# Performance work log

Measured on AMD Instinct MI355X. Metric: run time of the kernel, lower is better.

Reference implementation:

```python
import jax, jax.numpy as jnp
import numpy as np

S, B, LAG, H, F = 10, 16384, 5, 512, 5

def setup_inputs() -> dict:
    key = jax.random.key(0)
    ks = jax.random.split(key, 16)
    sc = 0.05
    inp = {
        'x': jax.random.normal(ks[0], (S, B, LAG), jnp.float32),
        'W_in': jax.random.normal(ks[1], (H, LAG), jnp.float32) * sc,
        'b_in': jax.random.normal(ks[2], (H,), jnp.float32) * sc,
        'Wih0': jax.random.normal(ks[3], (4 * H, H), jnp.float32) * sc,
        'Whh0': jax.random.normal(ks[4], (4 * H, H), jnp.float32) * sc,
        'bih0': jax.random.normal(ks[5], (4 * H,), jnp.float32) * sc,
        'bhh0': jax.random.normal(ks[6], (4 * H,), jnp.float32) * sc,
        'Wih1': jax.random.normal(ks[7], (4 * H, H), jnp.float32) * sc,
        'Whh1': jax.random.normal(ks[8], (4 * H, H), jnp.float32) * sc,
        'bih1': jax.random.normal(ks[9], (4 * H,), jnp.float32) * sc,
        'bhh1': jax.random.normal(ks[10], (4 * H,), jnp.float32) * sc,
        'W_out': jax.random.normal(ks[11], (1, H), jnp.float32) * sc,
        'b_out': jax.random.normal(ks[12], (1,), jnp.float32) * sc,
        'W_f': jax.random.normal(ks[13], (F, H), jnp.float32) * sc,
        'b_f': jax.random.normal(ks[14], (F,), jnp.float32) * sc,
    }
    return inp

def _lstm_cell(g, h, c, Whh, bhh):
    # g: precomputed input-side gates [B,4H]; add recurrent part, PyTorch gate order i,f,g,o
    g = g + h @ Whh.T + bhh
    i, f, gg, o = jnp.split(g, 4, axis=-1)
    c_new = jax.nn.sigmoid(f) * c + jax.nn.sigmoid(i) * jnp.tanh(gg)
    h_new = jax.nn.sigmoid(o) * jnp.tanh(c_new)
    return h_new, c_new

def reference(x, W_in, b_in, Wih0, Whh0, bih0, bhh0, Wih1, Whh1, bih1, bhh1, W_out, b_out, W_f, b_f):
    # input projection for all steps at once: [S,B,H]
    u = x @ W_in.T + b_in
    # precompute input-side LSTM gates for layer 0: [S,B,4H]
    g0_all = u @ Wih0.T + bih0
    zeros = jnp.zeros((B, H), x.dtype)

    def step(carry, g0_t):
        h0, c0, h1, c1 = carry
        h0, c0 = _lstm_cell(g0_t, h0, c0, Whh0, bhh0)
        g1 = h0 @ Wih1.T + bih1  # dropout between layers is eval-mode no-op
        h1, c1 = _lstm_cell(g1, h1, c1, Whh1, bhh1)
        return (h0, c0, h1, c1), h1

    (h0, c0, h1, c1), hs = jax.lax.scan(step, (zeros, zeros, zeros, zeros), g0_all)
    # per-step scalar outputs: [S,B,1] -> [B,S]
    step_out = (hs @ W_out.T + b_out)[:, :, 0].T
    # forecast head from last layer's final hidden state: [B,F]
    fc = h1 @ W_f.T + b_f
    outputs = jnp.concatenate([step_out, fc], axis=1)  # [B, S+F]
    h_n = jnp.stack([h0, h1])  # [2,B,H]
    c_n = jnp.stack([c0, c1])
    return outputs, h_n, c_n
```

## Files before the change

kernel.cpp:

```cpp
#include <hip/hip_runtime.h>
#include <hip/hip_bf16.h>

constexpr int S   = 10;
constexpr int Bsz = 16384;
constexpr int LAG = 5;
constexpr int H   = 512;
constexpr int G4  = 4 * H;
constexpr int F   = 5;
constexpr int BH  = Bsz * H;
constexpr int OUT_HN = Bsz * (S + F);
constexpr int OUT_CN = OUT_HN + 2 * BH;

constexpr int TK   = 32;
constexpr int NBUF = 2;
constexpr int A_T  = 128 * TK;
constexpr int B_T  = 128 * TK;

typedef __attribute__((ext_vector_type(8))) short short8;
typedef __attribute__((ext_vector_type(4))) float f32x4;

__device__ __forceinline__ float sigf(float x) { return 1.0f / (1.0f + __expf(-x)); }
__device__ __forceinline__ float tanh_fast(float x) {
    float e = __expf(2.0f * x);
    return 1.0f - 2.0f / (e + 1.0f);
}

__device__ __forceinline__ void gload_lds16(const void* g, void* l) {
    __builtin_amdgcn_global_load_lds(
        (const __attribute__((address_space(1))) unsigned int*)g,
        (__attribute__((address_space(3))) unsigned int*)l, 16, 0, 0);
}

__global__ __launch_bounds__(256)
void prep_kernel(const float* __restrict__ W_in,  const float* __restrict__ b_in,
                 const float* __restrict__ Wih0,  const float* __restrict__ Whh0,
                 const float* __restrict__ bih0,  const float* __restrict__ bhh0,
                 const float* __restrict__ Wih1,  const float* __restrict__ Whh1,
                 const float* __restrict__ bih1,  const float* __restrict__ bhh1,
                 __hip_bfloat16* __restrict__ W0b, __hip_bfloat16* __restrict__ W1b,
                 float* __restrict__ A0r, float* __restrict__ b0r,
                 float* __restrict__ b1r)
{
    const int r   = blockIdx.x;
    const int tid = threadIdx.x;

    for (int k = tid; k < H; k += 256)
        W0b[r * H + k] = __float2bfloat16(Whh0[r * H + k]);
    for (int k = tid; k < 2 * H; k += 256)
        W1b[r * 2 * H + k] = __float2bfloat16(
            (k < H) ? Wih1[r * H + k] : Whh1[r * H + (k - H)]);

    if (tid < LAG) {
        float s = 0.f;
        for (int h = 0; h < H; ++h) s += Wih0[r * H + h] * W_in[h * LAG + tid];
        A0r[r * LAG + tid] = s;
    } else if (tid == 5) {
        float s = 0.f;
        for (int h = 0; h < H; ++h) s += Wih0[r * H + h] * b_in[h];
        b0r[r] = s + bih0[r] + bhh0[r];
    } else if (tid == 6) {
        b1r[r] = bih1[r] + bhh1[r];
    }
}

__global__ __launch_bounds__(256)
void lstm_gemm(const __hip_bfloat16* __restrict__ Aseg0,
               const __hip_bfloat16* __restrict__ Aseg1,
               int nseg,
               const __hip_bfloat16* __restrict__ W, int ldw,
               const float* __restrict__ bias,
               const float* __restrict__ xs,
               const float* __restrict__ A0r,
               const float* __restrict__ c_in,
               float* __restrict__ c_out,
               float* __restrict__ h32_out,
               __hip_bfloat16* __restrict__ hb16_out,
               int hcol)
{
    __shared__ __align__(16) short As[NBUF * A_T];
    __shared__ __align__(16) short Bs[NBUF * B_T];
    __shared__ float xls[128 * LAG];
    __shared__ float a0ls[128 * LAG];

    const int tid  = threadIdx.x;
    const int lane = tid & 63;
    const int quad = lane >> 4;
    const int li   = lane & 15;
    const int wv   = tid >> 6;
    const int wy   = wv >> 1;
    const int wx   = wv & 1;

    const int l  = blockIdx.y * gridDim.x + blockIdx.x;
    const int v  = (l & 7) * 256 + (l >> 3);
    const int by = v >> 4;
    const int bx = v & 15;
    const int bM_ = by * 128;
    const int cn  = bx * 32;

    const bool has_x = (xs != nullptr);
    if (has_x) {
        for (int i = tid; i < 128 * LAG; i += 256) {
            const int row = i / LAG, ll = i % LAG;
            xls[i] = xs[(size_t)(bM_ + row) * LAG + ll];
        }
        for (int i = tid; i < 128 * LAG; i += 256) {
            const int cl = i / LAG, ll = i % LAG;
            const int r  = (cl >> 5) * H + cn + (cl & 31);
            a0ls[i] = A0r[r * LAG + ll];
        }
        __syncthreads();
    }

    f32x4 acc[4][4];
    #pragma unroll
    for (int i = 0; i < 4; ++i)
        #pragma unroll
        for (int j = 0; j < 4; ++j) acc[i][j] = (f32x4){0.f, 0.f, 0.f, 0.f};

    int a_off[2], w_off[2];
    #pragma unroll
    for (int r = 0; r < 2; ++r) {
        const int idx = r * 256 + tid;
        const int row = idx >> 2;
        const int j   = idx & 3;
        const int js  = j ^ ((row >> 1) & 3);
        a_off[r] = (bM_ + row) * 1024 + js * 8;
        const int rr = (row >> 5) * H + cn + (row & 31);
        w_off[r] = rr * ldw + js * 8;
    }

    const int NT = nseg * 16;

    auto stage_tile = [&](int t) {
        const int seg = t >> 4;
        const int kof = seg * 512 + (t & 15) * TK;
        const short* pa = (const short*)(seg ? Aseg1 : Aseg0) + kof;
        const short* pw = (const short*)W + kof;
        short* as = As + (t & 1) * A_T;
        short* bs = Bs + (t & 1) * B_T;
        #pragma unroll
        for (int r = 0; r < 2; ++r) {
            const int idx = r * 256 + tid;
            gload_lds16(pa + a_off[r], &as[idx * 8]);
            gload_lds16(pw + w_off[r], &bs[idx * 8]);
        }
    };

    const int pch = quad ^ ((li >> 1) & 3);

    auto compute_tile = [&](int t) {
        const short* as = As + (t & 1) * A_T;
        const short* bs = Bs + (t & 1) * B_T;
        short8 af[4], bf[4];
        #pragma unroll
        for (int m = 0; m < 4; ++m)
            af[m] = *(const short8*)&as[(wy * 64 + m * 16 + li) * TK + pch * 8];
        #pragma unroll
        for (int g = 0; g < 4; ++g)
            bf[g] = *(const short8*)&bs[(g * 32 + wx * 16 + li) * TK + pch * 8];
        __builtin_amdgcn_s_setprio(1);
        #pragma unroll
        for (int m = 0; m < 4; ++m)
            #pragma unroll
            for (int g = 0; g < 4; ++g)
                acc[m][g] = __builtin_amdgcn_mfma_f32_16x16x32_bf16(
                    af[m], bf[g], acc[m][g], 0, 0, 0);
        __builtin_amdgcn_s_setprio(0);
    };

    if (NT) {
        stage_tile(0);
        asm volatile("s_waitcnt vmcnt(0)\n\ts_barrier" ::: "memory");
        for (int t = 0; t < NT; ++t) {
            if (t + 1 < NT) stage_tile(t + 1);
            compute_tile(t);
            asm volatile("s_waitcnt vmcnt(0)\n\ts_barrier" ::: "memory");
        }
    }

    const int n = cn + wx * 16 + li;
    float bias4[4], a0reg[4][LAG];
    #pragma unroll
    for (int g = 0; g < 4; ++g) bias4[g] = bias[g * H + n];
    if (has_x) {
        #pragma unroll
        for (int g = 0; g < 4; ++g)
            #pragma unroll
            for (int ll = 0; ll < LAG; ++ll)
                a0reg[g][ll] = a0ls[(g * 32 + wx * 16 + li) * LAG + ll];
    }

    #pragma unroll
    for (int mt = 0; mt < 4; ++mt) {
        #pragma unroll
        for (int reg = 0; reg < 4; ++reg) {
            const int b_loc = wy * 64 + mt * 16 + quad * 4 + reg;
            const int b     = bM_ + b_loc;
            float g4[4];
            #pragma unroll
            for (int g = 0; g < 4; ++g) g4[g] = acc[mt][g][reg] + bias4[g];
            if (has_x) {
                #pragma unroll
                for (int ll = 0; ll < LAG; ++ll) {
                    const float xv = xls[b_loc * LAG + ll];
                    #pragma unroll
                    for (int g = 0; g < 4; ++g) g4[g] = fmaf(xv, a0reg[g][ll], g4[g]);
                }
            }
            const float ig = sigf(g4[0]);
            const float fg = sigf(g4[1]);
            const float gg = tanh_fast(g4[2]);
            const float og = sigf(g4[3]);
            const float cold = c_in ? c_in[(size_t)b * H + n] : 0.f;
            const float cnew = fg * cold + ig * gg;
            const float hh   = og * tanh_fast(cnew);
            c_out[(size_t)b * H + n] = cnew;
            if (h32_out) h32_out[(size_t)b * H + n] = hh;
            hb16_out[(size_t)b * 1024 + hcol + n] = __float2bfloat16(hh);
        }
    }
}

__global__ __launch_bounds__(256)
void out_head(const __hip_bfloat16* __restrict__ hcat,
              const float* __restrict__ W_out, const float* __restrict__ b_out,
              const float* __restrict__ W_f,   const float* __restrict__ b_f,
              float* __restrict__ out, int s, int last)
{
    const int wave = threadIdx.x >> 6;
    const int lane = threadIdx.x & 63;
    const int b    = blockIdx.x * 4 + wave;

    const __hip_bfloat16* hrow = hcat + (size_t)b * 1024 + 512;
    short8 hv = *(const short8*)&hrow[lane * 8];
    float h8[8];
    #pragma unroll
    for (int i = 0; i < 8; ++i) {
        union { unsigned int u; float f; } cv;
        cv.u = ((unsigned int)(unsigned short)hv[i]) << 16;
        h8[i] = cv.f;
    }

    {
        const float4 w0 = *reinterpret_cast<const float4*>(&W_out[lane * 8]);
        const float4 w1 = *reinterpret_cast<const float4*>(&W_out[lane * 8 + 4]);
        const float w8[8] = {w0.x, w0.y, w0.z, w0.w, w1.x, w1.y, w1.z, w1.w};
        float v = 0.f;
        #pragma unroll
        for (int i = 0; i < 8; ++i) v = fmaf(h8[i], w8[i], v);
        #pragma unroll
        for (int off = 32; off > 0; off >>= 1) v += __shfl_down(v, off, 64);
        if (lane == 0) out[b * (S + F) + s] = v + b_out[0];
    }
    if (last) {
        for (int f = 0; f < F; ++f) {
            const float4 w0 = *reinterpret_cast<const float4*>(&W_f[f * H + lane * 8]);
            const float4 w1 = *reinterpret_cast<const float4*>(&W_f[f * H + lane * 8 + 4]);
            const float w8[8] = {w0.x, w0.y, w0.z, w0.w, w1.x, w1.y, w1.z, w1.w};
            float v = 0.f;
            #pragma unroll
            for (int i = 0; i < 8; ++i) v = fmaf(h8[i], w8[i], v);
            #pragma unroll
            for (int off = 32; off > 0; off >>= 1) v += __shfl_down(v, off, 64);
            if (lane == 0) out[b * (S + F) + S + f] = v + b_f[f];
        }
    }
}

extern "C" void kernel_launch(void* const* d_in, const int* in_sizes, int n_in,
                              void* d_out, int out_size, void* d_ws, size_t ws_size,
                              hipStream_t stream)
{
    const float* x     = (const float*)d_in[0];
    const float* W_in  = (const float*)d_in[1];
    const float* b_in  = (const float*)d_in[2];
    const float* Wih0  = (const float*)d_in[3];
    const float* Whh0  = (const float*)d_in[4];
    const float* bih0  = (const float*)d_in[5];
    const float* bhh0  = (const float*)d_in[6];
    const float* Wih1  = (const float*)d_in[7];
    const float* Whh1  = (const float*)d_in[8];
    const float* bih1  = (const float*)d_in[9];
    const float* bhh1  = (const float*)d_in[10];
    const float* W_out = (const float*)d_in[11];
    const float* b_out = (const float*)d_in[12];
    const float* W_f   = (const float*)d_in[13];
    const float* b_f   = (const float*)d_in[14];

    float* out = (float*)d_out;
    char*  ws  = (char*)d_ws;

    __hip_bfloat16* hcat0 = (__hip_bfloat16*)ws;
    __hip_bfloat16* hcat1 = hcat0 + (size_t)Bsz * 1024;
    __hip_bfloat16* W0b   = hcat1 + (size_t)Bsz * 1024;
    __hip_bfloat16* W1b   = W0b + (size_t)G4 * H;
    float* A0r = (float*)(W1b + (size_t)G4 * 2 * H);
    float* b0r = A0r + G4 * LAG;
    float* b1r = b0r + G4;

    float* hn0 = out + OUT_HN;
    float* hn1 = out + OUT_HN + BH;
    float* c0  = out + OUT_CN;
    float* c1  = out + OUT_CN + BH;

    prep_kernel<<<dim3(G4), dim3(256), 0, stream>>>(
        W_in, b_in, Wih0, Whh0, bih0, bhh0, Wih1, Whh1, bih1, bhh1,
        W0b, W1b, A0r, b0r, b1r);

    __hip_bfloat16* hbuf[2] = {hcat0, hcat1};
    const dim3 grid(16, 128);
    const dim3 blk(256);

    for (int s = 0; s < S; ++s) {
        const bool first = (s == 0);
        const bool last  = (s == S - 1);
        __hip_bfloat16* cur  = hbuf[s & 1];
        __hip_bfloat16* prev = hbuf[(s + 1) & 1];

        lstm_gemm<<<grid, blk, 0, stream>>>(
            prev, nullptr, first ? 0 : 1, W0b, H, b0r,
            x + (size_t)s * Bsz * LAG, A0r,
            first ? nullptr : c0, c0, last ? hn0 : nullptr, cur, 0);

        lstm_gemm<<<grid, blk, 0, stream>>>(
            cur, prev, first ? 1 : 2, W1b, 2 * H, b1r,
            nullptr, nullptr,
            first ? nullptr : c1, c1, last ? hn1 : nullptr, cur, H);

        out_head<<<dim3(Bsz / 4), dim3(256), 0, stream>>>(
            cur, W_out, b_out, W_f, b_f, out, s, last ? 1 : 0);
    }
}
```

Measured before the change: 1.883 ms.

## Enlarge LSTM GEMM block tile to 256 rows with triple-buffered split staging

```diff
diff --git a/kernel.cpp b/kernel.cpp
--- a/kernel.cpp
+++ b/kernel.cpp
@@ -12,9 +12,11 @@
 constexpr int OUT_CN = OUT_HN + 2 * BH;
 
 constexpr int TK   = 32;
-constexpr int NBUF = 2;
-constexpr int A_T  = 128 * TK;
-constexpr int B_T  = 128 * TK;
+constexpr int NBUF = 3;
+constexpr int BM   = 256;
+constexpr int BNR  = 128;
+constexpr int A_T  = BM  * TK;
+constexpr int B_T  = BNR * TK;
 
 typedef __attribute__((ext_vector_type(8))) short short8;
 typedef __attribute__((ext_vector_type(4))) float f32x4;
@@ -63,7 +65,7 @@
     }
 }
 
-__global__ __launch_bounds__(256)
+__global__ __launch_bounds__(512, 4)
 void lstm_gemm(const __hip_bfloat16* __restrict__ Aseg0,
                const __hip_bfloat16* __restrict__ Aseg1,
                int nseg,
@@ -79,8 +81,8 @@
 {
     __shared__ __align__(16) short As[NBUF * A_T];
     __shared__ __align__(16) short Bs[NBUF * B_T];
-    __shared__ float xls[128 * LAG];
-    __shared__ float a0ls[128 * LAG];
+    __shared__ float xls[BM * LAG];
+    __shared__ float a0ls[BNR * LAG];
 
     const int tid  = threadIdx.x;
     const int lane = tid & 63;
@@ -91,19 +93,19 @@
     const int wx   = wv & 1;
 
     const int l  = blockIdx.y * gridDim.x + blockIdx.x;
-    const int v  = (l & 7) * 256 + (l >> 3);
+    const int v  = (l & 7) * 128 + (l >> 3);
     const int by = v >> 4;
     const int bx = v & 15;
-    const int bM_ = by * 128;
+    const int bM_ = by * BM;
     const int cn  = bx * 32;
 
     const bool has_x = (xs != nullptr);
     if (has_x) {
-        for (int i = tid; i < 128 * LAG; i += 256) {
+        for (int i = tid; i < BM * LAG; i += 512) {
             const int row = i / LAG, ll = i % LAG;
             xls[i] = xs[(size_t)(bM_ + row) * LAG + ll];
         }
-        for (int i = tid; i < 128 * LAG; i += 256) {
+        for (int i = tid; i < BNR * LAG; i += 512) {
             const int cl = i / LAG, ll = i % LAG;
             const int r  = (cl >> 5) * H + cn + (cl & 31);
             a0ls[i] = A0r[r * LAG + ll];
@@ -117,64 +119,90 @@
         #pragma unroll
         for (int j = 0; j < 4; ++j) acc[i][j] = (f32x4){0.f, 0.f, 0.f, 0.f};
 
-    int a_off[2], w_off[2];
+    int a_off[2], w_off;
     #pragma unroll
     for (int r = 0; r < 2; ++r) {
-        const int idx = r * 256 + tid;
+        const int idx = r * 512 + tid;
         const int row = idx >> 2;
         const int j   = idx & 3;
         const int js  = j ^ ((row >> 1) & 3);
         a_off[r] = (bM_ + row) * 1024 + js * 8;
-        const int rr = (row >> 5) * H + cn + (row & 31);
-        w_off[r] = rr * ldw + js * 8;
+    }
+    {
+        const int row = tid >> 2;
+        const int j   = tid & 3;
+        const int js  = j ^ ((row >> 1) & 3);
+        const int rr  = (row >> 5) * H + cn + (row & 31);
+        w_off = rr * ldw + js * 8;
     }
 
     const int NT = nseg * 16;
 
-    auto stage_tile = [&](int t) {
+    auto stage_A = [&](int t) {
         const int seg = t >> 4;
         const int kof = seg * 512 + (t & 15) * TK;
         const short* pa = (const short*)(seg ? Aseg1 : Aseg0) + kof;
+        short* as = As + (t % NBUF) * A_T;
+        #pragma unroll
+        for (int r = 0; r < 2; ++r)
+            gload_lds16(pa + a_off[r], &as[(r * 512 + tid) * 8]);
+    };
+    auto stage_B = [&](int t) {
+        const int seg = t >> 4;
+        const int kof = seg * 512 + (t & 15) * TK;
         const short* pw = (const short*)W + kof;
-        short* as = As + (t & 1) * A_T;
-        short* bs = Bs + (t & 1) * B_T;
-        #pragma unroll
-        for (int r = 0; r < 2; ++r) {
-            const int idx = r * 256 + tid;
-            gload_lds16(pa + a_off[r], &as[idx * 8]);
-            gload_lds16(pw + w_off[r], &bs[idx * 8]);
-        }
+        short* bs = Bs + (t % NBUF) * B_T;
+        gload_lds16(pw + w_off, &bs[tid * 8]);
     };
 
     const int pch = quad ^ ((li >> 1) & 3);
 
-    auto compute_tile = [&](int t) {
-        const short* as = As + (t & 1) * A_T;
-        const short* bs = Bs + (t & 1) * B_T;
-        short8 af[4], bf[4];
-        #pragma unroll
-        for (int m = 0; m < 4; ++m)
-            af[m] = *(const short8*)&as[(wy * 64 + m * 16 + li) * TK + pch * 8];
-        #pragma unroll
-        for (int g = 0; g < 4; ++g)
-            bf[g] = *(const short8*)&bs[(g * 32 + wx * 16 + li) * TK + pch * 8];
-        __builtin_amdgcn_s_setprio(1);
-        #pragma unroll
-        for (int m = 0; m < 4; ++m)
-            #pragma unroll
-            for (int g = 0; g < 4; ++g)
-                acc[m][g] = __builtin_amdgcn_mfma_f32_16x16x32_bf16(
-                    af[m], bf[g], acc[m][g], 0, 0, 0);
-        __builtin_amdgcn_s_setprio(0);
-    };
-
     if (NT) {
-        stage_tile(0);
-        asm volatile("s_waitcnt vmcnt(0)\n\ts_barrier" ::: "memory");
+        stage_A(0); stage_B(0);
+        stage_A(1); stage_B(1);
         for (int t = 0; t < NT; ++t) {
-            if (t + 1 < NT) stage_tile(t + 1);
-            compute_tile(t);
-            asm volatile("s_waitcnt vmcnt(0)\n\ts_barrier" ::: "memory");
+            if (t + 1 < NT) {
+                asm volatile("s_waitcnt vmcnt(3)\n\ts_barrier" ::: "memory");
+            } else {
+                asm volatile("s_waitcnt vmcnt(0)\n\ts_barrier" ::: "memory");
+            }
+            const short* as = As + (t % NBUF) * A_T;
+            const short* bs = Bs + (t % NBUF) * B_T;
+
+            short8 bf[4], af0, af1;
+            #pragma unroll
+            for (int g = 0; g < 4; ++g)
+                bf[g] = *(const short8*)&bs[(g * 32 + wx * 16 + li) * TK + pch * 8];
+            af0 = *(const short8*)&as[(wy * 64 + 0 * 16 + li) * TK + pch * 8];
+            af1 = *(const short8*)&as[(wy * 64 + 1 * 16 + li) * TK + pch * 8];
+            if (t + 2 < NT) stage_A(t + 2);
+            asm volatile("s_barrier" ::: "memory");
+            __builtin_amdgcn_s_setprio(1);
+            #pragma unroll
+            for (int g = 0; g < 4; ++g)
+                acc[0][g] = __builtin_amdgcn_mfma_f32_16x16x32_bf16(
+                    af0, bf[g], acc[0][g], 0, 0, 0);
+            #pragma unroll
+            for (int g = 0; g < 4; ++g)
+                acc[1][g] = __builtin_amdgcn_mfma_f32_16x16x32_bf16(
+                    af1, bf[g], acc[1][g], 0, 0, 0);
+            __builtin_amdgcn_s_setprio(0);
+
+            short8 af2, af3;
+            af2 = *(const short8*)&as[(wy * 64 + 2 * 16 + li) * TK + pch * 8];
+            af3 = *(const short8*)&as[(wy * 64 + 3 * 16 + li) * TK + pch * 8];
+            if (t + 2 < NT) stage_B(t + 2);
+            asm volatile("s_barrier" ::: "memory");
+            __builtin_amdgcn_s_setprio(1);
+            #pragma unroll
+            for (int g = 0; g < 4; ++g)
+                acc[2][g] = __builtin_amdgcn_mfma_f32_16x16x32_bf16(
+                    af2, bf[g], acc[2][g], 0, 0, 0);
+            #pragma unroll
+            for (int g = 0; g < 4; ++g)
+                acc[3][g] = __builtin_amdgcn_mfma_f32_16x16x32_bf16(
+                    af3, bf[g], acc[3][g], 0, 0, 0);
+            __builtin_amdgcn_s_setprio(0);
         }
     }
 
@@ -308,8 +336,8 @@
         W0b, W1b, A0r, b0r, b1r);
 
     __hip_bfloat16* hbuf[2] = {hcat0, hcat1};
-    const dim3 grid(16, 128);
-    const dim3 blk(256);
+    const dim3 grid(16, 64);
+    const dim3 blk(512);
 
     for (int s = 0; s < S; ++s) {
         const bool first = (s == 0);
```

Result: faster. 1.694 ms (-10.0%).

## Enlarge GEMM block to 256 rows, triple-buffer LDS, and template K-loop

Applied to the files above, without the earlier changes.

```diff
diff --git a/kernel.cpp b/kernel.cpp
--- a/kernel.cpp
+++ b/kernel.cpp
@@ -12,12 +12,24 @@
 constexpr int OUT_CN = OUT_HN + 2 * BH;
 
 constexpr int TK   = 32;
-constexpr int NBUF = 2;
-constexpr int A_T  = 128 * TK;
-constexpr int B_T  = 128 * TK;
+constexpr int NBUF = 3;
+constexpr int BM   = 256;
+constexpr int BNR  = 128;
+constexpr int A_T  = BM  * TK;
+constexpr int B_T  = BNR * TK;
 
 typedef __attribute__((ext_vector_type(8))) short short8;
 typedef __attribute__((ext_vector_type(4))) float f32x4;
+
+template <int I> struct Int { static constexpr int val = I; };
+
+template <int N, typename F>
+__device__ __forceinline__ void static_for(F&& f) {
+    if constexpr (N > 0) {
+        static_for<N - 1>(f);
+        f(Int<N - 1>{});
+    }
+}
 
 __device__ __forceinline__ float sigf(float x) { return 1.0f / (1.0f + __expf(-x)); }
 __device__ __forceinline__ float tanh_fast(float x) {
@@ -63,10 +75,9 @@
     }
 }
 
-__global__ __launch_bounds__(256)
-void lstm_gemm(const __hip_bfloat16* __restrict__ Aseg0,
-               const __hip_bfloat16* __restrict__ Aseg1,
-               int nseg,
+template <int NT>
+__global__ __launch_bounds__(512, 4)
+void lstm_gemm(const __hip_bfloat16* __restrict__ A,
                const __hip_bfloat16* __restrict__ W, int ldw,
                const float* __restrict__ bias,
                const float* __restrict__ xs,
@@ -79,8 +90,8 @@
 {
     __shared__ __align__(16) short As[NBUF * A_T];
     __shared__ __align__(16) short Bs[NBUF * B_T];
-    __shared__ float xls[128 * LAG];
-    __shared__ float a0ls[128 * LAG];
+    __shared__ float xls[BM * LAG];
+    __shared__ float a0ls[BNR * LAG];
 
     const int tid  = threadIdx.x;
     const int lane = tid & 63;
@@ -91,19 +102,19 @@
     const int wx   = wv & 1;
 
     const int l  = blockIdx.y * gridDim.x + blockIdx.x;
-    const int v  = (l & 7) * 256 + (l >> 3);
+    const int v  = (l & 7) * 128 + (l >> 3);
     const int by = v >> 4;
     const int bx = v & 15;
-    const int bM_ = by * 128;
+    const int bM_ = by * BM;
     const int cn  = bx * 32;
 
     const bool has_x = (xs != nullptr);
     if (has_x) {
-        for (int i = tid; i < 128 * LAG; i += 256) {
+        for (int i = tid; i < BM * LAG; i += 512) {
             const int row = i / LAG, ll = i % LAG;
             xls[i] = xs[(size_t)(bM_ + row) * LAG + ll];
         }
-        for (int i = tid; i < 128 * LAG; i += 256) {
+        for (int i = tid; i < BNR * LAG; i += 512) {
             const int cl = i / LAG, ll = i % LAG;
             const int r  = (cl >> 5) * H + cn + (cl & 31);
             a0ls[i] = A0r[r * LAG + ll];
@@ -117,65 +128,68 @@
         #pragma unroll
         for (int j = 0; j < 4; ++j) acc[i][j] = (f32x4){0.f, 0.f, 0.f, 0.f};
 
-    int a_off[2], w_off[2];
-    #pragma unroll
-    for (int r = 0; r < 2; ++r) {
-        const int idx = r * 256 + tid;
-        const int row = idx >> 2;
-        const int j   = idx & 3;
-        const int js  = j ^ ((row >> 1) & 3);
-        a_off[r] = (bM_ + row) * 1024 + js * 8;
-        const int rr = (row >> 5) * H + cn + (row & 31);
-        w_off[r] = rr * ldw + js * 8;
-    }
-
-    const int NT = nseg * 16;
-
-    auto stage_tile = [&](int t) {
-        const int seg = t >> 4;
-        const int kof = seg * 512 + (t & 15) * TK;
-        const short* pa = (const short*)(seg ? Aseg1 : Aseg0) + kof;
-        const short* pw = (const short*)W + kof;
-        short* as = As + (t & 1) * A_T;
-        short* bs = Bs + (t & 1) * B_T;
-        #pragma unroll
-        for (int r = 0; r < 2; ++r) {
-            const int idx = r * 256 + tid;
-            gload_lds16(pa + a_off[r], &as[idx * 8]);
-            gload_lds16(pw + w_off[r], &bs[idx * 8]);
-        }
-    };
-
-    const int pch = quad ^ ((li >> 1) & 3);
-
-    auto compute_tile = [&](int t) {
-        const short* as = As + (t & 1) * A_T;
-        const short* bs = Bs + (t & 1) * B_T;
-        short8 af[4], bf[4];
-        #pragma unroll
-        for (int m = 0; m < 4; ++m)
-            af[m] = *(const short8*)&as[(wy * 64 + m * 16 + li) * TK + pch * 8];
-        #pragma unroll
-        for (int g = 0; g < 4; ++g)
-            bf[g] = *(const short8*)&bs[(g * 32 + wx * 16 + li) * TK + pch * 8];
-        __builtin_amdgcn_s_setprio(1);
-        #pragma unroll
-        for (int m = 0; m < 4; ++m)
+    if constexpr (NT > 0) {
+        const short* Ab = (const short*)A;
+        const short* Wb = (const short*)W;
+        int a_off0, a_off1, w_off;
+        {
+            const int row0 = tid >> 2, j0 = tid & 3;
+            a_off0 = (bM_ + row0) * 1024 + (j0 ^ ((row0 >> 1) & 3)) * 8;
+            const int idx1 = 512 + tid;
+            const int row1 = idx1 >> 2, j1 = idx1 & 3;
+            a_off1 = (bM_ + row1) * 1024 + (j1 ^ ((row1 >> 1) & 3)) * 8;
+            const int rw = tid >> 2, jw = tid & 3;
+            const int rr = (rw >> 5) * H + cn + (rw & 31);
+            w_off = rr * ldw + (jw ^ ((rw >> 1) & 3)) * 8;
+        }
+        const int adst0 = tid * 8;
+        const int adst1 = (512 + tid) * 8;
+        const int bdst  = tid * 8;
+
+        auto stage = [&](auto tc) {
+            constexpr int t   = decltype(tc)::val;
+            constexpr int buf = t % NBUF;
+            gload_lds16(Ab + t * TK + a_off0, &As[buf * A_T + adst0]);
+            gload_lds16(Ab + t * TK + a_off1, &As[buf * A_T + adst1]);
+            gload_lds16(Wb + t * TK + w_off,  &Bs[buf * B_T + bdst]);
+        };
+
+        const int pch = quad ^ ((li >> 1) & 3);
+        const int arow = (wy * 64 + li) * TK + pch * 8;
+        const int brow = (wx * 16 + li) * TK + pch * 8;
+
+        stage(Int<0>{});
+        stage(Int<1>{});
+
+        static_for<NT>([&](auto tc) {
+            constexpr int t   = decltype(tc)::val;
+            constexpr int buf = t % NBUF;
+            if constexpr (t + 1 < NT)
+                asm volatile("s_waitcnt vmcnt(3)\n\ts_barrier" ::: "memory");
+            else
+                asm volatile("s_waitcnt vmcnt(0)\n\ts_barrier" ::: "memory");
+
+            const short* as = As + buf * A_T;
+            const short* bs = Bs + buf * B_T;
+            short8 af[4], bf[4];
+            #pragma unroll
+            for (int m = 0; m < 4; ++m)
+                af[m] = *(const short8*)&as[arow + m * 16 * TK];
             #pragma unroll
             for (int g = 0; g < 4; ++g)
-                acc[m][g] = __builtin_amdgcn_mfma_f32_16x16x32_bf16(
-                    af[m], bf[g], acc[m][g], 0, 0, 0);
-        __builtin_amdgcn_s_setprio(0);
-    };
-
-    if (NT) {
-        stage_tile(0);
-        asm volatile("s_waitcnt vmcnt(0)\n\ts_barrier" ::: "memory");
-        for (int t = 0; t < NT; ++t) {
-            if (t + 1 < NT) stage_tile(t + 1);
-            compute_tile(t);
-            asm volatile("s_waitcnt vmcnt(0)\n\ts_barrier" ::: "memory");
-        }
+                bf[g] = *(const short8*)&bs[brow + g * 32 * TK];
+
+            if constexpr (t + 2 < NT) stage(Int<t + 2>{});
+
+            __builtin_amdgcn_s_setprio(1);
+            #pragma unroll
+            for (int m = 0; m < 4; ++m)
+                #pragma unroll
+                for (int g = 0; g < 4; ++g)
+                    acc[m][g] = __builtin_amdgcn_mfma_f32_16x16x32_bf16(
+                        af[m], bf[g], acc[m][g], 0, 0, 0);
+            __builtin_amdgcn_s_setprio(0);
+        });
     }
 
     const int n = cn + wx * 16 + li;
@@ -308,26 +322,38 @@
         W0b, W1b, A0r, b0r, b1r);
 
     __hip_bfloat16* hbuf[2] = {hcat0, hcat1};
-    const dim3 grid(16, 128);
-    const dim3 blk(256);
+    const dim3 grid(16, 64);
+    const dim3 blk(512);
 
     for (int s = 0; s < S; ++s) {
         const bool first = (s == 0);
         const bool last  = (s == S - 1);
-        __hip_bfloat16* cur  = hbuf[s & 1];
-        __hip_bfloat16* prev = hbuf[(s + 1) & 1];
-
-        lstm_gemm<<<grid, blk, 0, stream>>>(
-            prev, nullptr, first ? 0 : 1, W0b, H, b0r,
-            x + (size_t)s * Bsz * LAG, A0r,
-            first ? nullptr : c0, c0, last ? hn0 : nullptr, cur, 0);
-
-        lstm_gemm<<<grid, blk, 0, stream>>>(
-            cur, prev, first ? 1 : 2, W1b, 2 * H, b1r,
-            nullptr, nullptr,
-            first ? nullptr : c1, c1, last ? hn1 : nullptr, cur, H);
+        __hip_bfloat16* cur = hbuf[s & 1];
+        __hip_bfloat16* nxt = hbuf[(s + 1) & 1];
+
+        if (first)
+            lstm_gemm<0><<<grid, blk, 0, stream>>>(
+                nullptr, W0b, H, b0r,
+                x + (size_t)s * Bsz * LAG, A0r,
+                nullptr, c0, nullptr, cur, 0);
+        else
+            lstm_gemm<16><<<grid, blk, 0, stream>>>(
+                nxt, W0b, H, b0r,
+                x + (size_t)s * Bsz * LAG, A0r,
+                c0, c0, last ? hn0 : nullptr, cur, 0);
+
+        if (first)
+            lstm_gemm<16><<<grid, blk, 0, stream>>>(
+                cur, W1b, 2 * H, b1r,
+                nullptr, nullptr,
+                nullptr, c1, nullptr, nxt, H);
+        else
+            lstm_gemm<32><<<grid, blk, 0, stream>>>(
+                cur, W1b, 2 * H, b1r,
+                nullptr, nullptr,
+                c1, c1, last ? hn1 : nullptr, nxt, H);
 
         out_head<<<dim3(Bsz / 4), dim3(256), 0, stream>>>(
-            cur, W_out, b_out, W_f, b_f, out, s, last ? 1 : 0);
-    }
-}
+            nxt, W_out, b_out, W_f, b_f, out, s, last ? 1 : 0);
+    }
+}
```

After: 1.651 ms. 1.14x faster.
